# Kernel optimization log

Measured on AMD Instinct MI355X. Metric: run time of the kernel, lower is better.

Reference implementation:

```python
import jax, jax.numpy as jnp
import numpy as np

N, H = 8192, 256
TOP_K = 16          # k = min(top_k, N-1)
TEMPERATURE = 1.0
NEG_SLOPE = 0.2
NUM_SECTORS = 11


def setup_inputs() -> dict:
    key = jax.random.key(0)
    kE, kW, ka, ks, kA = jax.random.split(key, 5)
    embeddings = jax.random.normal(kE, (N, H), dtype=jnp.float32)
    # xavier-uniform-like scale for W (nn.Linear, bias=False)
    lim = float(np.sqrt(6.0 / (H + H)))
    W = jax.random.uniform(kW, (H, H), dtype=jnp.float32, minval=-lim, maxval=lim)
    # a ~ Normal(0, 1/sqrt(2H))
    a = jax.random.normal(ka, (2 * H,), dtype=jnp.float32) * (1.0 / np.sqrt(2 * H))
    sector_ids = jax.random.randint(ks, (N,), 0, NUM_SECTORS, dtype=jnp.int32)
    active_mask = jax.random.randint(kA, (N,), 0, 2, dtype=jnp.int32).astype(bool)
    return {"embeddings": embeddings, "W": W, "a": a,
            "sector_ids": sector_ids, "active_mask": active_mask}


def reference(embeddings, W, a, sector_ids, active_mask):
    # h = W(embeddings)  (torch Linear: x @ W.T)
    h = embeddings @ W.T                                   # [N, H]
    # attention[i,j] = leaky_relu(a . [h_i, h_j]) = leaky_relu(a1.h_i + a2.h_j)
    # (decomposition of the concat+matmul; same math, avoids O(N^2*2H) tensor)
    a1, a2 = a[:H], a[H:]
    s_i = h @ a1                                           # [N]
    s_j = h @ a2                                           # [N]
    att = jax.nn.leaky_relu(s_i[:, None] + s_j[None, :], NEG_SLOPE) / TEMPERATURE
    # combined mask: active pairs AND same sector
    mask = (active_mask[:, None] & active_mask[None, :]) \
           & (sector_ids[:, None] == sector_ids[None, :])  # [N, N]
    att = jnp.where(mask, att, -jnp.inf)
    k = min(TOP_K, N - 1)
    topk_values, topk_indices = jax.lax.top_k(att, k)      # [N, k] each
    valid = jnp.isfinite(topk_values)                      # invalid = masked-out slots
    # dense padded representation of (edge_index, edge_weight):
    # src = topk_indices, dst = row index, weight = topk_values where valid
    edge_weight = jnp.where(valid, topk_values, 0.0)
    return edge_weight, topk_indices, valid
```

## Files before the change

### kernel.cpp

```cpp
#include <hip/hip_runtime.h>

#define N 8192
#define H 256
#define TOPK 16
#define NSEC 11
#define NEG_SLOPE 0.2
#define NB 256
#define NT 256
#define RPB (N / NB)
#define NSL 8
#define SLICE (N / NSL)
#define IDX_SENT 0x7fffffff

__device__ __forceinline__ bool better(double av, int ai, double bv, int bi) {
    return (av > bv) || (av == bv && ai < bi);
}

__global__ __launch_bounds__(NT) void compute_v_s(
    const float* __restrict__ E, const float* __restrict__ W,
    const float* __restrict__ a,
    float* __restrict__ s1f, double* __restrict__ s2g)
{
    __shared__ float sa[2 * H];
    __shared__ double sv1[H];
    __shared__ double sv2[H];

    int t = threadIdx.x;
    int blk = blockIdx.x;
    int lane = t & 63;
    int w = t >> 6;

    sa[t] = a[t];
    sa[t + H] = a[t + H];
    __syncthreads();

    {
        double a1_0 = 0.0, a1_1 = 0.0, a1_2 = 0.0, a1_3 = 0.0;
        double a2_0 = 0.0, a2_1 = 0.0, a2_2 = 0.0, a2_3 = 0.0;
        for (int j = 0; j < H; j += 4) {
            double w0 = (double)W[(j + 0) * H + t];
            double w1 = (double)W[(j + 1) * H + t];
            double w2 = (double)W[(j + 2) * H + t];
            double w3 = (double)W[(j + 3) * H + t];
            a1_0 += w0 * (double)sa[j + 0];
            a1_1 += w1 * (double)sa[j + 1];
            a1_2 += w2 * (double)sa[j + 2];
            a1_3 += w3 * (double)sa[j + 3];
            a2_0 += w0 * (double)sa[H + j + 0];
            a2_1 += w1 * (double)sa[H + j + 1];
            a2_2 += w2 * (double)sa[H + j + 2];
            a2_3 += w3 * (double)sa[H + j + 3];
        }
        sv1[t] = (a1_0 + a1_1) + (a1_2 + a1_3);
        sv2[t] = (a2_0 + a2_1) + (a2_2 + a2_3);
    }
    __syncthreads();

    {
        float4 e[RPB / 4];
#pragma unroll
        for (int q = 0; q < RPB / 4; ++q) {
            int row = blk * RPB + (w + 4 * q);
            e[q] = ((const float4*)(E + (size_t)row * H))[lane];
        }
        int base = lane * 4;
        double b10 = sv1[base + 0], b11 = sv1[base + 1],
               b12 = sv1[base + 2], b13 = sv1[base + 3];
        double b20 = sv2[base + 0], b21 = sv2[base + 1],
               b22 = sv2[base + 2], b23 = sv2[base + 3];
#pragma unroll
        for (int q = 0; q < RPB / 4; ++q) {
            int row = blk * RPB + (w + 4 * q);
            double acc1 = (double)e[q].x * b10 + (double)e[q].y * b11 +
                          (double)e[q].z * b12 + (double)e[q].w * b13;
            double acc2 = (double)e[q].x * b20 + (double)e[q].y * b21 +
                          (double)e[q].z * b22 + (double)e[q].w * b23;
            for (int o = 32; o > 0; o >>= 1) {
                acc1 += __shfl_down(acc1, o);
                acc2 += __shfl_down(acc2, o);
            }
            if (lane == 0) {
                s1f[row] = (float)acc1;
                s2g[row] = acc2;
            }
        }
    }
}

__global__ __launch_bounds__(NT) void slice_topk(
    const double* __restrict__ s2g, const int* __restrict__ sec,
    const int* __restrict__ act,
    double* __restrict__ candV, int* __restrict__ candI,
    int* __restrict__ cnts)
{
    __shared__ double wV[4][TOPK];
    __shared__ int wI[4][TOPK];
    __shared__ int wCnt[4];

    int bx = blockIdx.x;
    int c = bx >> 3;
    int sl = bx & 7;
    int t = threadIdx.x;
    int lane = t & 63;
    int w = t >> 6;

    int j0 = sl * SLICE + 4 * t;
    int4 a4 = *(const int4*)(act + j0);
    int4 s4 = *(const int4*)(sec + j0);
    double2 d01 = *(const double2*)(s2g + j0);
    double2 d23 = *(const double2*)(s2g + j0 + 2);

    bool p0 = (a4.x != 0) && (s4.x == c);
    bool p1 = (a4.y != 0) && (s4.y == c);
    bool p2 = (a4.z != 0) && (s4.z == c);
    bool p3 = (a4.w != 0) && (s4.w == c);

    double v[4];
    int ix[4];
    v[0] = p0 ? d01.x : -INFINITY;  ix[0] = p0 ? (j0 + 0) : IDX_SENT;
    v[1] = p1 ? d01.y : -INFINITY;  ix[1] = p1 ? (j0 + 1) : IDX_SENT;
    v[2] = p2 ? d23.x : -INFINITY;  ix[2] = p2 ? (j0 + 2) : IDX_SENT;
    v[3] = p3 ? d23.y : -INFINITY;  ix[3] = p3 ? (j0 + 3) : IDX_SENT;

    int cnt = __popcll(__ballot(p0)) + __popcll(__ballot(p1)) +
              __popcll(__ballot(p2)) + __popcll(__ballot(p3));

    for (int r = 0; r < TOPK; ++r) {
        double bv = v[0];
        int bi = ix[0];
#pragma unroll
        for (int p = 1; p < 4; ++p)
            if (better(v[p], ix[p], bv, bi)) { bv = v[p]; bi = ix[p]; }
        for (int o = 32; o > 0; o >>= 1) {
            double ov = __shfl_xor(bv, o);
            int oi = __shfl_xor(bi, o);
            if (better(ov, oi, bv, bi)) { bv = ov; bi = oi; }
        }
#pragma unroll
        for (int p = 0; p < 4; ++p)
            if (ix[p] == bi) { v[p] = -INFINITY; ix[p] = IDX_SENT; }
        if (lane == 0) {
            wV[w][r] = bv;
            wI[w][r] = bi;
        }
    }
    if (lane == 0) wCnt[w] = cnt;
    __syncthreads();

    if (w == 0) {
        double mv = wV[lane >> 4][lane & 15];
        int mi = wI[lane >> 4][lane & 15];
        for (int r = 0; r < TOPK; ++r) {
            double bv = mv;
            int bi = mi;
            for (int o = 32; o > 0; o >>= 1) {
                double ov = __shfl_xor(bv, o);
                int oi = __shfl_xor(bi, o);
                if (better(ov, oi, bv, bi)) { bv = ov; bi = oi; }
            }
            if (mi == bi) { mv = -INFINITY; mi = IDX_SENT; }
            if (lane == 0) {
                candV[bx * TOPK + r] = bv;
                candI[bx * TOPK + r] = bi;
            }
        }
        if (lane == 0) cnts[bx] = wCnt[0] + wCnt[1] + wCnt[2] + wCnt[3];
    }
}

__global__ __launch_bounds__(64) void merge_topk(
    const double* __restrict__ candV, const int* __restrict__ candI,
    const int* __restrict__ cnts, const int* __restrict__ sec,
    const int* __restrict__ act,
    int* __restrict__ top_idx, int* __restrict__ fill_idx,
    int* __restrict__ m_arr)
{
    int c = blockIdx.x;
    int lane = threadIdx.x;

    const double* cbV = candV + (size_t)c * NSL * TOPK;
    const int* cbI = candI + (size_t)c * NSL * TOPK;
    double v0 = cbV[lane];
    int i0 = cbI[lane];
    double v1 = cbV[lane + 64];
    int i1 = cbI[lane + 64];

    for (int r = 0; r < TOPK; ++r) {
        double bv;
        int bi;
        if (better(v0, i0, v1, i1)) { bv = v0; bi = i0; }
        else                        { bv = v1; bi = i1; }
        for (int o = 32; o > 0; o >>= 1) {
            double ov = __shfl_xor(bv, o);
            int oi = __shfl_xor(bi, o);
            if (better(ov, oi, bv, bi)) { bv = ov; bi = oi; }
        }
        if (i0 == bi)      { v0 = -INFINITY; i0 = IDX_SENT; }
        else if (i1 == bi) { v1 = -INFINITY; i1 = IDX_SENT; }
        if (lane == 0) top_idx[c * TOPK + r] = (bi == IDX_SENT) ? -1 : bi;
    }

    int cl = (lane < NSL) ? cnts[c * NSL + lane] : 0;
    for (int o = 32; o > 0; o >>= 1) cl += __shfl_xor(cl, o);
    if (lane == 0) m_arr[c] = (cl < TOPK) ? cl : TOPK;

    int cnt2 = 0;
    for (int basej = 0; basej < N && cnt2 < TOPK; basej += 64) {
        int j = basej + lane;
        bool fail = !((act[j] != 0) && (sec[j] == c));
        unsigned long long mask = __ballot(fail);
        if (fail) {
            int rank = cnt2 + __popcll(mask & ((1ull << lane) - 1));
            if (rank < TOPK) fill_idx[c * TOPK + rank] = j;
        }
        cnt2 += __popcll(mask);
    }
}

__global__ __launch_bounds__(NT) void write_out(const float* __restrict__ s1f,
                                                const double* __restrict__ s2g,
                                                const int* __restrict__ sec,
                                                const int* __restrict__ act,
                                                const int* __restrict__ top_idx,
                                                const int* __restrict__ fill_idx,
                                                const int* __restrict__ m_arr,
                                                float* __restrict__ out) {
    int gid = blockIdx.x * NT + threadIdx.x;
    int i = gid >> 4;
    int slot = gid & 15;

    float wgt = 0.0f;
    float fidx;
    float fvalid = 0.0f;

    if (act[i] == 0) {
        fidx = (float)slot;
    } else {
        int c = sec[i];
        int m = m_arr[c];
        if (slot < m) {
            int j = top_idx[c * TOPK + slot];
            double x = (double)s1f[i] + s2g[j];
            double attv = (x >= 0.0) ? x : NEG_SLOPE * x;
            wgt = (float)attv;
            fvalid = 1.0f;
            fidx = (float)j;
        } else {
            fidx = (float)fill_idx[c * TOPK + (slot - m)];
        }
    }

    out[gid] = wgt;
    out[N * TOPK + gid] = fidx;
    out[2 * N * TOPK + gid] = fvalid;
}

extern "C" void kernel_launch(void* const* d_in, const int* in_sizes, int n_in,
                              void* d_out, int out_size, void* d_ws, size_t ws_size,
                              hipStream_t stream) {
    const float* E = (const float*)d_in[0];
    const float* W = (const float*)d_in[1];
    const float* a = (const float*)d_in[2];
    const int* sec = (const int*)d_in[3];
    const int* act = (const int*)d_in[4];

    char* ws = (char*)d_ws;
    double* s2g = (double*)ws;
    double* candV = s2g + N;
    float* s1f = (float*)(candV + NSEC * NSL * TOPK);
    int* candI = (int*)(s1f + N);
    int* cnts = candI + NSEC * NSL * TOPK;
    int* top_idx = cnts + NSEC * NSL;
    int* fill_idx = top_idx + NSEC * TOPK;
    int* m_arr = fill_idx + NSEC * TOPK;

    float* out = (float*)d_out;

    hipLaunchKernelGGL(compute_v_s, dim3(NB), dim3(NT), 0, stream,
                       E, W, a, s1f, s2g);
    hipLaunchKernelGGL(slice_topk, dim3(NSEC * NSL), dim3(NT), 0, stream,
                       s2g, sec, act, candV, candI, cnts);
    hipLaunchKernelGGL(merge_topk, dim3(NSEC), dim3(64), 0, stream,
                       candV, candI, cnts, sec, act, top_idx, fill_idx, m_arr);
    hipLaunchKernelGGL(write_out, dim3((N * TOPK) / NT), dim3(NT), 0, stream,
                       s1f, s2g, sec, act, top_idx, fill_idx, m_arr, out);
}
```

Baseline: 110.9 us.

## Fuse slice top-k, merge and output write into one kernel via last-block arrival

Replaces the slice_topk, merge_topk and write_out launches with a single fused kernel. The last slice block of each sector, found with an atomic arrival counter, performs the merge and then writes all output rows for its sector. Inactive rows are written by the sector-0 blocks. This removes two kernel launches and their global round-trips, but the output writes now run on only 11 blocks, each looping over all N rows with scalar, strided stores, which may serialize poorly.

```diff
diff --git a/kernel.cpp b/kernel.cpp
--- a/kernel.cpp
+++ b/kernel.cpp
@@ -19,7 +19,8 @@
 __global__ __launch_bounds__(NT) void compute_v_s(
     const float* __restrict__ E, const float* __restrict__ W,
     const float* __restrict__ a,
-    float* __restrict__ s1f, double* __restrict__ s2g)
+    float* __restrict__ s1f, double* __restrict__ s2g,
+    int* __restrict__ arrive)
 {
     __shared__ float sa[2 * H];
     __shared__ double sv1[H];
@@ -29,6 +30,8 @@
     int blk = blockIdx.x;
     int lane = t & 63;
     int w = t >> 6;
+
+    if (blk == 0 && t < NSEC) arrive[t] = 0;
 
     sa[t] = a[t];
     sa[t + H] = a[t + H];
@@ -87,15 +90,22 @@
     }
 }
 
-__global__ __launch_bounds__(NT) void slice_topk(
-    const double* __restrict__ s2g, const int* __restrict__ sec,
-    const int* __restrict__ act,
+__global__ __launch_bounds__(NT) void fused_topk(
+    const float* __restrict__ s1f, const double* __restrict__ s2g,
+    const int* __restrict__ sec, const int* __restrict__ act,
     double* __restrict__ candV, int* __restrict__ candI,
-    int* __restrict__ cnts)
+    int* __restrict__ cnts, int* __restrict__ arrive,
+    float* __restrict__ out)
 {
     __shared__ double wV[4][TOPK];
     __shared__ int wI[4][TOPK];
     __shared__ int wCnt[4];
+    __shared__ int sLast;
+    __shared__ int sTopI[TOPK];
+    __shared__ double sD[TOPK];
+    __shared__ float sFidx[TOPK];
+    __shared__ float sFill[TOPK];
+    __shared__ int sM;
 
     int bx = blockIdx.x;
     int c = bx >> 3;
@@ -124,6 +134,26 @@
 
     int cnt = __popcll(__ballot(p0)) + __popcll(__ballot(p1)) +
               __popcll(__ballot(p2)) + __popcll(__ballot(p3));
+
+    if (c == 0) {
+        int av[4] = {a4.x, a4.y, a4.z, a4.w};
+#pragma unroll
+        for (int p = 0; p < 4; ++p) {
+            if (av[p] == 0) {
+                int rown = j0 + p;
+                float4* o0 = (float4*)(out + (size_t)rown * TOPK);
+                float4* o1 = (float4*)(out + (size_t)N * TOPK + (size_t)rown * TOPK);
+                float4* o2 = (float4*)(out + 2 * (size_t)N * TOPK + (size_t)rown * TOPK);
+                float4 z = make_float4(0.f, 0.f, 0.f, 0.f);
+                o0[0] = z; o0[1] = z; o0[2] = z; o0[3] = z;
+                o1[0] = make_float4(0.f, 1.f, 2.f, 3.f);
+                o1[1] = make_float4(4.f, 5.f, 6.f, 7.f);
+                o1[2] = make_float4(8.f, 9.f, 10.f, 11.f);
+                o1[3] = make_float4(12.f, 13.f, 14.f, 15.f);
+                o2[0] = z; o2[1] = z; o2[2] = z; o2[3] = z;
+            }
+        }
+    }
 
     for (int r = 0; r < TOPK; ++r) {
         double bv = v[0];
@@ -164,95 +194,88 @@
                 candI[bx * TOPK + r] = bi;
             }
         }
-        if (lane == 0) cnts[bx] = wCnt[0] + wCnt[1] + wCnt[2] + wCnt[3];
-    }
-}
-
-__global__ __launch_bounds__(64) void merge_topk(
-    const double* __restrict__ candV, const int* __restrict__ candI,
-    const int* __restrict__ cnts, const int* __restrict__ sec,
-    const int* __restrict__ act,
-    int* __restrict__ top_idx, int* __restrict__ fill_idx,
-    int* __restrict__ m_arr)
-{
-    int c = blockIdx.x;
-    int lane = threadIdx.x;
-
-    const double* cbV = candV + (size_t)c * NSL * TOPK;
-    const int* cbI = candI + (size_t)c * NSL * TOPK;
-    double v0 = cbV[lane];
-    int i0 = cbI[lane];
-    double v1 = cbV[lane + 64];
-    int i1 = cbI[lane + 64];
-
-    for (int r = 0; r < TOPK; ++r) {
-        double bv;
-        int bi;
-        if (better(v0, i0, v1, i1)) { bv = v0; bi = i0; }
-        else                        { bv = v1; bi = i1; }
-        for (int o = 32; o > 0; o >>= 1) {
-            double ov = __shfl_xor(bv, o);
-            int oi = __shfl_xor(bi, o);
-            if (better(ov, oi, bv, bi)) { bv = ov; bi = oi; }
-        }
-        if (i0 == bi)      { v0 = -INFINITY; i0 = IDX_SENT; }
-        else if (i1 == bi) { v1 = -INFINITY; i1 = IDX_SENT; }
-        if (lane == 0) top_idx[c * TOPK + r] = (bi == IDX_SENT) ? -1 : bi;
-    }
-
-    int cl = (lane < NSL) ? cnts[c * NSL + lane] : 0;
-    for (int o = 32; o > 0; o >>= 1) cl += __shfl_xor(cl, o);
-    if (lane == 0) m_arr[c] = (cl < TOPK) ? cl : TOPK;
-
-    int cnt2 = 0;
-    for (int basej = 0; basej < N && cnt2 < TOPK; basej += 64) {
-        int j = basej + lane;
-        bool fail = !((act[j] != 0) && (sec[j] == c));
-        unsigned long long mask = __ballot(fail);
-        if (fail) {
-            int rank = cnt2 + __popcll(mask & ((1ull << lane) - 1));
-            if (rank < TOPK) fill_idx[c * TOPK + rank] = j;
-        }
-        cnt2 += __popcll(mask);
-    }
-}
-
-__global__ __launch_bounds__(NT) void write_out(const float* __restrict__ s1f,
-                                                const double* __restrict__ s2g,
-                                                const int* __restrict__ sec,
-                                                const int* __restrict__ act,
-                                                const int* __restrict__ top_idx,
-                                                const int* __restrict__ fill_idx,
-                                                const int* __restrict__ m_arr,
-                                                float* __restrict__ out) {
-    int gid = blockIdx.x * NT + threadIdx.x;
-    int i = gid >> 4;
-    int slot = gid & 15;
-
-    float wgt = 0.0f;
-    float fidx;
-    float fvalid = 0.0f;
-
-    if (act[i] == 0) {
-        fidx = (float)slot;
-    } else {
-        int c = sec[i];
-        int m = m_arr[c];
-        if (slot < m) {
-            int j = top_idx[c * TOPK + slot];
-            double x = (double)s1f[i] + s2g[j];
-            double attv = (x >= 0.0) ? x : NEG_SLOPE * x;
-            wgt = (float)attv;
-            fvalid = 1.0f;
-            fidx = (float)j;
-        } else {
-            fidx = (float)fill_idx[c * TOPK + (slot - m)];
-        }
-    }
-
-    out[gid] = wgt;
-    out[N * TOPK + gid] = fidx;
-    out[2 * N * TOPK + gid] = fvalid;
+        if (lane == 0) {
+            cnts[bx] = wCnt[0] + wCnt[1] + wCnt[2] + wCnt[3];
+            __threadfence();
+            int old = atomicAdd(&arrive[c], 1);
+            sLast = (old == NSL - 1);
+        }
+    }
+    __syncthreads();
+    if (!sLast) return;
+
+    __threadfence();
+
+    if (w == 0) {
+        const double* cbV = candV + (size_t)c * NSL * TOPK;
+        const int* cbI = candI + (size_t)c * NSL * TOPK;
+        double v0 = cbV[lane];
+        int i0 = cbI[lane];
+        double v1 = cbV[lane + 64];
+        int i1 = cbI[lane + 64];
+        for (int r = 0; r < TOPK; ++r) {
+            double bv;
+            int bi;
+            if (better(v0, i0, v1, i1)) { bv = v0; bi = i0; }
+            else                        { bv = v1; bi = i1; }
+            for (int o = 32; o > 0; o >>= 1) {
+                double ov = __shfl_xor(bv, o);
+                int oi = __shfl_xor(bi, o);
+                if (better(ov, oi, bv, bi)) { bv = ov; bi = oi; }
+            }
+            if (i0 == bi)      { v0 = -INFINITY; i0 = IDX_SENT; }
+            else if (i1 == bi) { v1 = -INFINITY; i1 = IDX_SENT; }
+            if (lane == 0) sTopI[r] = bi;
+        }
+        int cl = (lane < NSL) ? cnts[c * NSL + lane] : 0;
+        for (int o = 32; o > 0; o >>= 1) cl += __shfl_xor(cl, o);
+        if (lane == 0) sM = (cl < TOPK) ? cl : TOPK;
+    } else if (w == 1) {
+        int cnt2 = 0;
+        for (int basej = 0; basej < N && cnt2 < TOPK; basej += 64) {
+            int j = basej + lane;
+            bool fail = !((act[j] != 0) && (sec[j] == c));
+            unsigned long long mask = __ballot(fail);
+            if (fail) {
+                int rank = cnt2 + __popcll(mask & ((1ull << lane) - 1));
+                if (rank < TOPK) sFill[rank] = (float)j;
+            }
+            cnt2 += __popcll(mask);
+        }
+    }
+    __syncthreads();
+
+    if (t < TOPK) {
+        int j = sTopI[t];
+        sD[t] = (j == IDX_SENT) ? 0.0 : s2g[j];
+        sFidx[t] = (j == IDX_SENT) ? 0.0f : (float)j;
+    }
+    __syncthreads();
+
+    int mm = sM;
+    for (int i = t; i < N; i += NT) {
+        if (act[i] != 0 && sec[i] == c) {
+            double s1d = (double)s1f[i];
+#pragma unroll
+            for (int slot = 0; slot < TOPK; ++slot) {
+                float wgt, fidx, fvalid;
+                if (slot < mm) {
+                    double x = s1d + sD[slot];
+                    double attv = (x >= 0.0) ? x : NEG_SLOPE * x;
+                    wgt = (float)attv;
+                    fvalid = 1.0f;
+                    fidx = sFidx[slot];
+                } else {
+                    wgt = 0.0f;
+                    fvalid = 0.0f;
+                    fidx = sFill[slot - mm];
+                }
+                out[(size_t)i * TOPK + slot] = wgt;
+                out[(size_t)N * TOPK + (size_t)i * TOPK + slot] = fidx;
+                out[2 * (size_t)N * TOPK + (size_t)i * TOPK + slot] = fvalid;
+            }
+        }
+    }
 }
 
 extern "C" void kernel_launch(void* const* d_in, const int* in_sizes, int n_in,
@@ -270,18 +293,12 @@
     float* s1f = (float*)(candV + NSEC * NSL * TOPK);
     int* candI = (int*)(s1f + N);
     int* cnts = candI + NSEC * NSL * TOPK;
-    int* top_idx = cnts + NSEC * NSL;
-    int* fill_idx = top_idx + NSEC * TOPK;
-    int* m_arr = fill_idx + NSEC * TOPK;
+    int* arrive = cnts + NSEC * NSL;
 
     float* out = (float*)d_out;
 
     hipLaunchKernelGGL(compute_v_s, dim3(NB), dim3(NT), 0, stream,
-                       E, W, a, s1f, s2g);
-    hipLaunchKernelGGL(slice_topk, dim3(NSEC * NSL), dim3(NT), 0, stream,
-                       s2g, sec, act, candV, candI, cnts);
-    hipLaunchKernelGGL(merge_topk, dim3(NSEC), dim3(64), 0, stream,
-                       candV, candI, cnts, sec, act, top_idx, fill_idx, m_arr);
-    hipLaunchKernelGGL(write_out, dim3((N * TOPK) / NT), dim3(NT), 0, stream,
-                       s1f, s2g, sec, act, top_idx, fill_idx, m_arr, out);
+                       E, W, a, s1f, s2g, arrive);
+    hipLaunchKernelGGL(fused_topk, dim3(NSEC * NSL), dim3(NT), 0, stream,
+                       s1f, s2g, sec, act, candV, candI, cnts, arrive, out);
 }
```

New measurement: 181.8 us. 63.9% more time.

## Fuse per-sector merge into slice top-k via last-block atomic arrival

Applied to the files above, without the earlier changes.

Removes the separate merge_topk launch: each slice block increments a per-sector arrival counter after writing its candidates, and the last block to arrive does the per-sector merge. The fill-index scan now runs on a second wavefront in parallel with the top-k merge instead of after it. Counters are reset in the first kernel. This saves one kernel launch and its gap, at the cost of threadfence/atomic synchronization and reliance on that reset.

```diff
diff --git a/kernel.cpp b/kernel.cpp
--- a/kernel.cpp
+++ b/kernel.cpp
@@ -19,7 +19,8 @@
 __global__ __launch_bounds__(NT) void compute_v_s(
     const float* __restrict__ E, const float* __restrict__ W,
     const float* __restrict__ a,
-    float* __restrict__ s1f, double* __restrict__ s2g)
+    float* __restrict__ s1f, double* __restrict__ s2g,
+    int* __restrict__ arrive)
 {
     __shared__ float sa[2 * H];
     __shared__ double sv1[H];
@@ -29,6 +30,8 @@
     int blk = blockIdx.x;
     int lane = t & 63;
     int w = t >> 6;
+
+    if (blk == 0 && t < NSEC) arrive[t] = 0;
 
     sa[t] = a[t];
     sa[t + H] = a[t + H];
@@ -87,15 +90,18 @@
     }
 }
 
-__global__ __launch_bounds__(NT) void slice_topk(
+__global__ __launch_bounds__(NT) void slice_merge(
     const double* __restrict__ s2g, const int* __restrict__ sec,
     const int* __restrict__ act,
     double* __restrict__ candV, int* __restrict__ candI,
-    int* __restrict__ cnts)
+    int* __restrict__ cnts, int* __restrict__ arrive,
+    int* __restrict__ top_idx, int* __restrict__ fill_idx,
+    int* __restrict__ m_arr)
 {
     __shared__ double wV[4][TOPK];
     __shared__ int wI[4][TOPK];
     __shared__ int wCnt[4];
+    __shared__ int sLast;
 
     int bx = blockIdx.x;
     int c = bx >> 3;
@@ -164,56 +170,54 @@
                 candI[bx * TOPK + r] = bi;
             }
         }
-        if (lane == 0) cnts[bx] = wCnt[0] + wCnt[1] + wCnt[2] + wCnt[3];
-    }
-}
-
-__global__ __launch_bounds__(64) void merge_topk(
-    const double* __restrict__ candV, const int* __restrict__ candI,
-    const int* __restrict__ cnts, const int* __restrict__ sec,
-    const int* __restrict__ act,
-    int* __restrict__ top_idx, int* __restrict__ fill_idx,
-    int* __restrict__ m_arr)
-{
-    int c = blockIdx.x;
-    int lane = threadIdx.x;
-
-    const double* cbV = candV + (size_t)c * NSL * TOPK;
-    const int* cbI = candI + (size_t)c * NSL * TOPK;
-    double v0 = cbV[lane];
-    int i0 = cbI[lane];
-    double v1 = cbV[lane + 64];
-    int i1 = cbI[lane + 64];
-
-    for (int r = 0; r < TOPK; ++r) {
-        double bv;
-        int bi;
-        if (better(v0, i0, v1, i1)) { bv = v0; bi = i0; }
-        else                        { bv = v1; bi = i1; }
-        for (int o = 32; o > 0; o >>= 1) {
-            double ov = __shfl_xor(bv, o);
-            int oi = __shfl_xor(bi, o);
-            if (better(ov, oi, bv, bi)) { bv = ov; bi = oi; }
-        }
-        if (i0 == bi)      { v0 = -INFINITY; i0 = IDX_SENT; }
-        else if (i1 == bi) { v1 = -INFINITY; i1 = IDX_SENT; }
-        if (lane == 0) top_idx[c * TOPK + r] = (bi == IDX_SENT) ? -1 : bi;
-    }
-
-    int cl = (lane < NSL) ? cnts[c * NSL + lane] : 0;
-    for (int o = 32; o > 0; o >>= 1) cl += __shfl_xor(cl, o);
-    if (lane == 0) m_arr[c] = (cl < TOPK) ? cl : TOPK;
-
-    int cnt2 = 0;
-    for (int basej = 0; basej < N && cnt2 < TOPK; basej += 64) {
-        int j = basej + lane;
-        bool fail = !((act[j] != 0) && (sec[j] == c));
-        unsigned long long mask = __ballot(fail);
-        if (fail) {
-            int rank = cnt2 + __popcll(mask & ((1ull << lane) - 1));
-            if (rank < TOPK) fill_idx[c * TOPK + rank] = j;
-        }
-        cnt2 += __popcll(mask);
+        if (lane == 0) {
+            cnts[bx] = wCnt[0] + wCnt[1] + wCnt[2] + wCnt[3];
+            __threadfence();
+            int old = atomicAdd(&arrive[c], 1);
+            sLast = (old == NSL - 1);
+        }
+    }
+    __syncthreads();
+    if (!sLast) return;
+
+    __threadfence();
+
+    if (w == 0) {
+        const double* cbV = candV + (size_t)c * NSL * TOPK;
+        const int* cbI = candI + (size_t)c * NSL * TOPK;
+        double v0 = cbV[lane];
+        int i0 = cbI[lane];
+        double v1 = cbV[lane + 64];
+        int i1 = cbI[lane + 64];
+        for (int r = 0; r < TOPK; ++r) {
+            double bv;
+            int bi;
+            if (better(v0, i0, v1, i1)) { bv = v0; bi = i0; }
+            else                        { bv = v1; bi = i1; }
+            for (int o = 32; o > 0; o >>= 1) {
+                double ov = __shfl_xor(bv, o);
+                int oi = __shfl_xor(bi, o);
+                if (better(ov, oi, bv, bi)) { bv = ov; bi = oi; }
+            }
+            if (i0 == bi)      { v0 = -INFINITY; i0 = IDX_SENT; }
+            else if (i1 == bi) { v1 = -INFINITY; i1 = IDX_SENT; }
+            if (lane == 0) top_idx[c * TOPK + r] = (bi == IDX_SENT) ? -1 : bi;
+        }
+        int cl = (lane < NSL) ? cnts[c * NSL + lane] : 0;
+        for (int o = 32; o > 0; o >>= 1) cl += __shfl_xor(cl, o);
+        if (lane == 0) m_arr[c] = (cl < TOPK) ? cl : TOPK;
+    } else if (w == 1) {
+        int cnt2 = 0;
+        for (int basej = 0; basej < N && cnt2 < TOPK; basej += 64) {
+            int j = basej + lane;
+            bool fail = !((act[j] != 0) && (sec[j] == c));
+            unsigned long long mask = __ballot(fail);
+            if (fail) {
+                int rank = cnt2 + __popcll(mask & ((1ull << lane) - 1));
+                if (rank < TOPK) fill_idx[c * TOPK + rank] = j;
+            }
+            cnt2 += __popcll(mask);
+        }
     }
 }
 
@@ -273,15 +277,15 @@
     int* top_idx = cnts + NSEC * NSL;
     int* fill_idx = top_idx + NSEC * TOPK;
     int* m_arr = fill_idx + NSEC * TOPK;
+    int* arrive = m_arr + NSEC;
 
     float* out = (float*)d_out;
 
     hipLaunchKernelGGL(compute_v_s, dim3(NB), dim3(NT), 0, stream,
-                       E, W, a, s1f, s2g);
-    hipLaunchKernelGGL(slice_topk, dim3(NSEC * NSL), dim3(NT), 0, stream,
-                       s2g, sec, act, candV, candI, cnts);
-    hipLaunchKernelGGL(merge_topk, dim3(NSEC), dim3(64), 0, stream,
-                       candV, candI, cnts, sec, act, top_idx, fill_idx, m_arr);
+                       E, W, a, s1f, s2g, arrive);
+    hipLaunchKernelGGL(slice_merge, dim3(NSEC * NSL), dim3(NT), 0, stream,
+                       s2g, sec, act, candV, candI, cnts, arrive,
+                       top_idx, fill_idx, m_arr);
     hipLaunchKernelGGL(write_out, dim3((N * TOPK) / NT), dim3(NT), 0, stream,
                        s1f, s2g, sec, act, top_idx, fill_idx, m_arr, out);
 }
```

After: 113.4 us. 1.02x slower.
